# Kernel tuning notes

Measured on AMD Instinct MI355X. Metric: run time of the kernel, lower is better.

## Reference

```python
import jax, jax.numpy as jnp
import numpy as np

NUM_HEADS = 4
NUM_GROUPS = 8
EPS = 1e-5


def group_norm(x, w, b):
    # x: (B, C, H, W); normalize per group of C//NUM_GROUPS channels
    B, C, H, W = x.shape
    xg = x.reshape(B, NUM_GROUPS, C // NUM_GROUPS, H, W)
    mean = xg.mean(axis=(2, 3, 4), keepdims=True)
    var = xg.var(axis=(2, 3, 4), keepdims=True)
    xn = ((xg - mean) * jax.lax.rsqrt(var + EPS)).reshape(B, C, H, W)
    return xn * w[None, :, None, None] + b[None, :, None, None]


def conv1x1(x, w, b):
    # x: (B, C_in, H, W), w: (C_out, C_in), b: (C_out,)
    return jnp.einsum('bchw,oc->bohw', x, w) + b[None, :, None, None]


def setup_inputs() -> dict:
    key = jax.random.key(0)
    B, C, H, W = 4, 256, 64, 64
    k1, k2, k3 = jax.random.split(key, 3)
    scale = 1.0 / np.sqrt(C)
    return {
        'x': jax.random.normal(k1, (B, C, H, W), dtype=jnp.float32),
        'norm_w': jnp.ones((C,), dtype=jnp.float32),
        'norm_b': jnp.zeros((C,), dtype=jnp.float32),
        'qkv_w': jax.random.normal(k2, (3 * C, C), dtype=jnp.float32) * scale,
        'qkv_b': jnp.zeros((3 * C,), dtype=jnp.float32),
        'proj_w': jax.random.normal(k3, (C, C), dtype=jnp.float32) * scale,
        'proj_b': jnp.zeros((C,), dtype=jnp.float32),
    }


def reference(x, norm_w, norm_b, qkv_w, qkv_b, proj_w, proj_b):
    B, C, H, W = x.shape
    hd = C // NUM_HEADS  # head dim
    h = group_norm(x, norm_w, norm_b)
    qkv = conv1x1(h, qkv_w, qkv_b)            # (B, 3C, H, W)
    q, k, v = jnp.split(qkv, 3, axis=1)
    q = q.reshape(B, NUM_HEADS, hd, H * W)
    k = k.reshape(B, NUM_HEADS, hd, H * W)
    v = v.reshape(B, NUM_HEADS, hd, H * W)
    attn = jnp.einsum('bhcn,bhcm->bhnm', q, k) / jnp.sqrt(jnp.asarray(hd, x.dtype))
    attn = jax.nn.softmax(attn, axis=-1)
    out = jnp.einsum('bhnm,bhcm->bhcn', attn, v).reshape(B, C, H, W)
    out = conv1x1(out, proj_w, proj_b)
    return x + out
```

## Files before the change

kernel.cpp:

```cpp
#include <hip/hip_runtime.h>
#include <hip/hip_bf16.h>
#include <stdint.h>


#define B_  4
#define C_  256
#define N_  4096
#define NH_ 4
#define HD_ 64
#define G_  8
#define CPG_ 32
#define GRP_ELEMS (CPG_ * N_)

typedef __attribute__((ext_vector_type(8))) short short8;
typedef __attribute__((ext_vector_type(4))) float f32x4;
typedef __attribute__((ext_vector_type(4))) unsigned short us4;

__device__ __forceinline__ unsigned short f2bf(float f) {
  union { float f; unsigned u; } v; v.f = f;
  unsigned r = v.u + 0x7FFFu + ((v.u >> 16) & 1u);
  return (unsigned short)(r >> 16);
}

__device__ __forceinline__ unsigned pkbf2(float a, float b) {
  __hip_bfloat162 h = __float22bfloat162_rn(make_float2(a, b));
  unsigned r; __builtin_memcpy(&r, &h, sizeof(r)); return r;
}

__device__ __forceinline__ void dma16(const unsigned short* g, unsigned short* l) {
  __builtin_amdgcn_global_load_lds(
      (const __attribute__((address_space(1))) unsigned int*)(g),
      (__attribute__((address_space(3))) unsigned int*)(l), 16, 0, 0);
}

__global__ void gn_partial_cvt(const float* __restrict__ x, float* __restrict__ partial,
                               const float* __restrict__ qkvw, const float* __restrict__ projw,
                               unsigned short* __restrict__ wq, unsigned short* __restrict__ wp) {
  __shared__ float ls[8];
  int t = threadIdx.x;
  if (blockIdx.x >= 512) {
    int i = (blockIdx.x - 512) * 256 + t;
    if (i < 768 * 256) wq[i] = f2bf(qkvw[i]);
    if (i < 256 * 256) wp[i] = f2bf(projw[i]);
    return;
  }
  int idx = blockIdx.x;
  int slice = idx & 15, g = (idx >> 4) & 7, b = idx >> 7;
  const float* base = x + (size_t)(b * C_ + g * CPG_) * N_ + slice * 256;
  float s = 0.f, sq = 0.f;
#pragma unroll
  for (int cc = 0; cc < CPG_; cc++) {
    float v = base[(size_t)cc * N_ + t];
    s += v; sq += v * v;
  }
#pragma unroll
  for (int off = 32; off; off >>= 1) {
    s  += __shfl_down(s,  off, 64);
    sq += __shfl_down(sq, off, 64);
  }
  int wave = t >> 6, lane = t & 63;
  if (lane == 0) { ls[wave * 2] = s; ls[wave * 2 + 1] = sq; }
  __syncthreads();
  if (t == 0) {
    float S = ls[0] + ls[2] + ls[4] + ls[6];
    float SQ = ls[1] + ls[3] + ls[5] + ls[7];
    partial[idx * 2] = S; partial[idx * 2 + 1] = SQ;
  }
}

__global__ void gn_apply(const float* __restrict__ x,
                         const float* __restrict__ nw, const float* __restrict__ nb,
                         const float* __restrict__ partial, unsigned short* __restrict__ hT) {
  int nt = blockIdx.x, ct = blockIdx.y, b = blockIdx.z;
  __shared__ unsigned short tile[32][72];
  int t = threadIdx.x;
  int lane = t & 63;
  int grp = b * G_ + ct;
  float s = 0.f, sq = 0.f;
  if (lane < 16) {
    s  = partial[(grp * 16 + lane) * 2];
    sq = partial[(grp * 16 + lane) * 2 + 1];
  }
#pragma unroll
  for (int off = 8; off; off >>= 1) {
    s  += __shfl_down(s,  off, 64);
    sq += __shfl_down(sq, off, 64);
  }
  s  = __shfl(s,  0, 64);
  sq = __shfl(sq, 0, 64);
  const float inv = 1.0f / (float)GRP_ELEMS;
  float mean = s * inv;
  float rstd = rsqrtf(sq * inv - mean * mean + 1e-5f);

  int n_loc = t & 63, c_loc = t >> 6;
  const float* xb = x + (size_t)(b * C_ + ct * CPG_) * N_ + nt * 64;
#pragma unroll
  for (int rr = 0; rr < 8; rr++) {
    int cc = rr * 4 + c_loc;
    int c = ct * CPG_ + cc;
    float v = xb[(size_t)cc * N_ + n_loc];
    v = (v - mean) * rstd * nw[c] + nb[c];
    tile[cc][n_loc] = f2bf(v);
  }
  __syncthreads();
  int n = t >> 2, c8 = (t & 3) * 8;
  us4 lo, hi;
#pragma unroll
  for (int j = 0; j < 4; j++) lo[j] = tile[c8 + j][n];
#pragma unroll
  for (int j = 0; j < 4; j++) hi[j] = tile[c8 + 4 + j][n];
  unsigned short* outp = hT + ((size_t)(b * N_ + nt * 64 + n)) * C_ + ct * CPG_ + c8;
  *reinterpret_cast<us4*>(outp) = lo;
  *reinterpret_cast<us4*>(outp + 4) = hi;
}

__global__ __launch_bounds__(256) void qkv_gemm(
    const unsigned short* __restrict__ hT, const unsigned short* __restrict__ wq,
    const float* __restrict__ qb,
    unsigned short* __restrict__ Qt, unsigned short* __restrict__ Kt,
    unsigned short* __restrict__ V) {
  int ot = blockIdx.x >> 7;
  int nt = (blockIdx.x & 127) >> 2;
  int b  = blockIdx.x & 3;
  int t = threadIdx.x;
  int wave = t >> 6, lane = t & 63, l15 = lane & 15, quad = lane >> 4, l7 = l15 & 7;

  __shared__ __align__(16) unsigned short sh[128 * C_];
  {
    int row0 = wave * 2 + (lane >> 5);
    int col8 = lane & 31;
    int src8 = (col8 & 24) | ((col8 & 7) ^ (row0 & 7));
    const unsigned short* gsrc = hT + ((size_t)(b * N_ + nt * 128 + row0)) * C_ + src8 * 8;
#pragma unroll
    for (int it = 0; it < 16; it++)
      dma16(gsrc + (size_t)it * 8 * C_, sh + (it * 8 + wave * 2) * C_);
  }

  f32x4 acc[2][8];
#pragma unroll
  for (int r = 0; r < 2; r++)
#pragma unroll
    for (int tt = 0; tt < 8; tt++) acc[r][tt] = (f32x4){0.f, 0.f, 0.f, 0.f};

  const short8* arow[2];
#pragma unroll
  for (int r = 0; r < 2; r++)
    arow[r] = reinterpret_cast<const short8*>(
        wq + (size_t)(ot * 128 + wave * 32 + r * 16 + l15) * C_);

  asm volatile("s_waitcnt vmcnt(0)" ::: "memory");
  __syncthreads();

#pragma unroll
  for (int kk = 0; kk < 8; kk++) {
    int g = kk * 4 + quad;
    int col8 = (g & 24) | ((g & 7) ^ l7);
    short8 bfr[8];
#pragma unroll
    for (int tt = 0; tt < 8; tt++)
      bfr[tt] = *reinterpret_cast<const short8*>(&sh[(tt * 16 + l15) * C_ + col8 * 8]);
#pragma unroll
    for (int r = 0; r < 2; r++) {
      short8 a = arow[r][g];
#pragma unroll
      for (int tt = 0; tt < 8; tt++)
        acc[r][tt] = __builtin_amdgcn_mfma_f32_16x16x32_bf16(a, bfr[tt], acc[r][tt], 0, 0, 0);
    }
  }

  int sec = ot >> 1;
  int head = (ot & 1) * 2 + (wave >> 1);
  int bh = b * NH_ + head;
  const float SC = 0.125f * 1.44269504088896340736f;

#pragma unroll
  for (int r = 0; r < 2; r++) {
    int o_glob = ot * 128 + wave * 32 + r * 16;
    int cw = (o_glob & 63) + quad * 4;
    if (sec == 0) {
#pragma unroll
      for (int tt = 0; tt < 8; tt++) {
        int n = nt * 128 + tt * 16 + l15;
        us4 pk;
#pragma unroll
        for (int i = 0; i < 4; i++)
          pk[i] = f2bf((acc[r][tt][i] + qb[o_glob + quad * 4 + i]) * SC);
        *reinterpret_cast<us4*>(Qt + ((size_t)bh * N_ + n) * HD_ + cw) = pk;
      }
    } else if (sec == 1) {
#pragma unroll
      for (int tt = 0; tt < 8; tt++) {
        int n = nt * 128 + tt * 16 + l15;
        us4 pk;
#pragma unroll
        for (int i = 0; i < 4; i++)
          pk[i] = f2bf(acc[r][tt][i] + qb[o_glob + quad * 4 + i]);
        *reinterpret_cast<us4*>(Kt + ((size_t)bh * N_ + n) * HD_ + cw) = pk;
      }
    } else {
#pragma unroll
      for (int tt = 0; tt < 8; tt++) {
        int n = nt * 128 + tt * 16 + l15;
#pragma unroll
        for (int i = 0; i < 4; i++)
          V[((size_t)bh * HD_ + cw + i) * N_ + n] =
              f2bf(acc[r][tt][i] + qb[o_glob + quad * 4 + i]);
      }
    }
  }
}

__global__ __launch_bounds__(256, 2) void flash_attn(
    const unsigned short* __restrict__ Qt, const unsigned short* __restrict__ Kt,
    const unsigned short* __restrict__ Vv, unsigned short* __restrict__ aoT) {
  int bh = blockIdx.x & 15, qt = blockIdx.x >> 4;
  int b = bh >> 2, head = bh & 3;
  int t = threadIdx.x;
  int wave = t >> 6, lane = t & 63, l15 = lane & 15, quad = lane >> 4;
  int l7 = l15 & 7;
  int qsub = wave >> 1, khalf = wave & 1;

  const unsigned short* Qb = Qt + (size_t)bh * N_ * HD_;
  const unsigned short* Kb = Kt + (size_t)bh * N_ * HD_;
  const unsigned short* Vb = Vv + (size_t)bh * HD_ * N_;
  int q_base = qt * 128 + qsub * 64;

  __shared__ __align__(16) unsigned char smem[65536];
  unsigned short* Ks = (unsigned short*)smem;
  unsigned short* Vs = (unsigned short*)(smem + 32768);
  float* Obuf = (float*)smem;
  float* lbuf = (float*)(smem + 34816);

  const short8 vones = {(short)0x3F80, (short)0x3F80, (short)0x3F80, (short)0x3F80,
                        (short)0x3F80, (short)0x3F80, (short)0x3F80, (short)0x3F80};

  short8 qf[4][2];
#pragma unroll
  for (int r = 0; r < 4; r++)
#pragma unroll
    for (int h = 0; h < 2; h++)
      qf[r][h] = *reinterpret_cast<const short8*>(
          Qb + (size_t)(q_base + r * 16 + l15) * HD_ + h * 32 + quad * 8);

  f32x4 oa[4][4], la[4];
#pragma unroll
  for (int r = 0; r < 4; r++) {
    la[r] = (f32x4){0.f, 0.f, 0.f, 0.f};
#pragma unroll
    for (int ct = 0; ct < 4; ct++) oa[r][ct] = (f32x4){0.f, 0.f, 0.f, 0.f};
  }

  int i8 = lane >> 3, e = lane & 7;
  int perm = (e ^ i8) * 8;
  int kvoff = (khalf * 2) * 4096;
  auto stage = [&](int kt2, int buf) {
    int m0 = khalf * 2048 + kt2 * 64;
    unsigned short* Kd = Ks + kvoff + buf * 4096;
    unsigned short* Vd = Vs + kvoff + buf * 4096;
#pragma unroll
    for (int cc = 0; cc < 4; cc++) {
      int c = qsub * 4 + cc;
      dma16(Kb + (size_t)(m0 + c * 8 + i8) * HD_ + perm, Kd + c * 512);
      dma16(Vb + (size_t)(c * 8 + i8) * N_ + m0 + perm, Vd + c * 512);
    }
  };

  stage(0, 0);

#pragma unroll 1
  for (int kt = 0; kt < 32; kt++) {
    int buf = kt & 1;
    if (kt + 1 < 32) {
      stage(kt + 1, buf ^ 1);
      asm volatile("s_waitcnt vmcnt(8)" ::: "memory");
    } else {
      asm volatile("s_waitcnt vmcnt(0)" ::: "memory");
    }
    __builtin_amdgcn_s_barrier();

    const unsigned short* Kbuf = Ks + kvoff + buf * 4096;
    const unsigned short* Vbuf = Vs + kvoff + buf * 4096;

    short8 kf[4][2], vf[4][2];
#pragma unroll
    for (int tt = 0; tt < 4; tt++)
#pragma unroll
      for (int kh2 = 0; kh2 < 2; kh2++) {
        kf[tt][kh2] = *reinterpret_cast<const short8*>(
            &Kbuf[(tt * 16 + l15) * 64 + (((kh2 * 4 + quad) ^ l7) * 8)]);
        vf[tt][kh2] = *reinterpret_cast<const short8*>(
            &Vbuf[(tt * 16 + l15) * 64 + (((kh2 * 4 + quad) ^ l7) * 8)]);
      }

#pragma unroll
    for (int r = 0; r < 4; r++) {
      f32x4 s[4];
#pragma unroll
      for (int tt = 0; tt < 4; tt++) {
        f32x4 z = (f32x4){0.f, 0.f, 0.f, 0.f};
        z = __builtin_amdgcn_mfma_f32_16x16x32_bf16(kf[tt][0], qf[r][0], z, 0, 0, 0);
        s[tt] = __builtin_amdgcn_mfma_f32_16x16x32_bf16(kf[tt][1], qf[r][1], z, 0, 0, 0);
      }
      unsigned Apk[4], Bpk[4];
#pragma unroll
      for (int tt = 0; tt < 4; tt++) {
        Apk[tt] = pkbf2(__builtin_amdgcn_exp2f(s[tt][0]), __builtin_amdgcn_exp2f(s[tt][1]));
        Bpk[tt] = pkbf2(__builtin_amdgcn_exp2f(s[tt][2]), __builtin_amdgcn_exp2f(s[tt][3]));
      }
      union { unsigned u[4]; short8 v; } f0, f1;
      {
        auto ua = __builtin_amdgcn_permlane32_swap(Apk[0], Apk[1], false, false);
        auto pa = __builtin_amdgcn_permlane16_swap(ua[0], ua[1], false, false);
        auto ub = __builtin_amdgcn_permlane32_swap(Bpk[0], Bpk[1], false, false);
        auto pb = __builtin_amdgcn_permlane16_swap(ub[0], ub[1], false, false);
        f0.u[0] = pa[0]; f0.u[1] = pb[0]; f0.u[2] = pa[1]; f0.u[3] = pb[1];
        auto uc = __builtin_amdgcn_permlane32_swap(Apk[2], Apk[3], false, false);
        auto pc = __builtin_amdgcn_permlane16_swap(uc[0], uc[1], false, false);
        auto ud = __builtin_amdgcn_permlane32_swap(Bpk[2], Bpk[3], false, false);
        auto pd = __builtin_amdgcn_permlane16_swap(ud[0], ud[1], false, false);
        f1.u[0] = pc[0]; f1.u[1] = pd[0]; f1.u[2] = pc[1]; f1.u[3] = pd[1];
      }
      short8 pf0 = f0.v, pf1 = f1.v;
#pragma unroll
      for (int ct = 0; ct < 4; ct++) {
        oa[r][ct] = __builtin_amdgcn_mfma_f32_16x16x32_bf16(vf[ct][0], pf0, oa[r][ct], 0, 0, 0);
        oa[r][ct] = __builtin_amdgcn_mfma_f32_16x16x32_bf16(vf[ct][1], pf1, oa[r][ct], 0, 0, 0);
      }
      la[r] = __builtin_amdgcn_mfma_f32_16x16x32_bf16(vones, pf0, la[r], 0, 0, 0);
      la[r] = __builtin_amdgcn_mfma_f32_16x16x32_bf16(vones, pf1, la[r], 0, 0, 0);
    }
  }

  __builtin_amdgcn_s_barrier();
  if (khalf == 1) {
#pragma unroll
    for (int r = 0; r < 4; r++) {
#pragma unroll
      for (int ct = 0; ct < 4; ct++)
#pragma unroll
        for (int i = 0; i < 4; i++)
          Obuf[qsub * 4352 + (ct * 16 + quad * 4 + i) * 68 + r * 16 + l15] = oa[r][ct][i];
      if (quad == 0) lbuf[qsub * 64 + r * 16 + l15] = la[r][0];
    }
  }
  __builtin_amdgcn_s_barrier();
  if (khalf == 0) {
#pragma unroll
    for (int r = 0; r < 4; r++) {
      float inv = 1.0f / (la[r][0] + lbuf[qsub * 64 + r * 16 + l15]);
      int n = q_base + r * 16 + l15;
#pragma unroll
      for (int ct = 0; ct < 4; ct++) {
        const float* ob = &Obuf[qsub * 4352 + (ct * 16 + quad * 4) * 68 + r * 16 + l15];
        union { unsigned u2[2]; us4 v; } w;
        w.u2[0] = pkbf2((oa[r][ct][0] + ob[0]) * inv, (oa[r][ct][1] + ob[68]) * inv);
        w.u2[1] = pkbf2((oa[r][ct][2] + ob[136]) * inv, (oa[r][ct][3] + ob[204]) * inv);
        *reinterpret_cast<us4*>(
            aoT + ((size_t)(b * N_ + n)) * C_ + head * HD_ + ct * 16 + quad * 4) = w.v;
      }
    }
  }
}

__global__ __launch_bounds__(256) void proj_gemm(
    const unsigned short* __restrict__ aoT, const unsigned short* __restrict__ wp,
    const float* __restrict__ pb, const float* __restrict__ x,
    float* __restrict__ out) {
  int ot = blockIdx.x >> 7;
  int nt = (blockIdx.x & 127) >> 2;
  int b  = blockIdx.x & 3;
  int t = threadIdx.x;
  int wave = t >> 6, lane = t & 63, l15 = lane & 15, quad = lane >> 4, l7 = l15 & 7;
  int o_base = ot * 64 + wave * 16;

  __shared__ __align__(16) unsigned short sh[128 * C_];
  {
    int row0 = wave * 2 + (lane >> 5);
    int col8 = lane & 31;
    int src8 = (col8 & 24) | ((col8 & 7) ^ (row0 & 7));
    const unsigned short* gsrc = aoT + ((size_t)(b * N_ + nt * 128 + row0)) * C_ + src8 * 8;
#pragma unroll
    for (int it = 0; it < 16; it++)
      dma16(gsrc + (size_t)it * 8 * C_, sh + (it * 8 + wave * 2) * C_);
  }

  f32x4 acc[8];
#pragma unroll
  for (int tt = 0; tt < 8; tt++) acc[tt] = (f32x4){0.f, 0.f, 0.f, 0.f};

  const short8* arow = reinterpret_cast<const short8*>(wp + (size_t)(o_base + l15) * C_);

  asm volatile("s_waitcnt vmcnt(0)" ::: "memory");
  __syncthreads();

#pragma unroll
  for (int kk = 0; kk < 8; kk++) {
    short8 a = arow[kk * 4 + quad];
    int g = kk * 4 + quad;
    int col8 = (g & 24) | ((g & 7) ^ l7);
#pragma unroll
    for (int tt = 0; tt < 8; tt++) {
      short8 bf = *reinterpret_cast<const short8*>(&sh[(tt * 16 + l15) * C_ + col8 * 8]);
      acc[tt] = __builtin_amdgcn_mfma_f32_16x16x32_bf16(a, bf, acc[tt], 0, 0, 0);
    }
  }
#pragma unroll
  for (int tt = 0; tt < 8; tt++) {
    int n = nt * 128 + tt * 16 + l15;
#pragma unroll
    for (int i = 0; i < 4; i++) {
      int o = o_base + quad * 4 + i;
      size_t idx = ((size_t)(b * C_ + o)) * N_ + n;
      out[idx] = acc[tt][i] + pb[o] + x[idx];
    }
  }
}

extern "C" void kernel_launch(void* const* d_in, const int* in_sizes, int n_in,
                              void* d_out, int out_size, void* d_ws, size_t ws_size,
                              hipStream_t stream) {
  const float* x      = (const float*)d_in[0];
  const float* norm_w = (const float*)d_in[1];
  const float* norm_b = (const float*)d_in[2];
  const float* qkv_w  = (const float*)d_in[3];
  const float* qkv_b  = (const float*)d_in[4];
  const float* proj_w = (const float*)d_in[5];
  const float* proj_b = (const float*)d_in[6];
  float* out = (float*)d_out;

  char* ws = (char*)d_ws;
  size_t off = 0;
  auto alloc = [&](size_t bytes) { size_t o = off; off = (off + bytes + 255) & ~(size_t)255; return o; };
  size_t off_partial = alloc(512 * 2 * sizeof(float));
  size_t off_stats   = alloc(32 * 2 * sizeof(float));
  size_t off_wq      = alloc((size_t)768 * 256 * 2);
  size_t off_wp      = alloc((size_t)256 * 256 * 2);
  size_t off_hT      = alloc((size_t)B_ * N_ * C_ * 2);
  size_t off_Qt      = alloc((size_t)B_ * NH_ * N_ * HD_ * 2);
  size_t off_Kt      = alloc((size_t)B_ * NH_ * N_ * HD_ * 2);
  size_t off_V       = alloc((size_t)B_ * NH_ * HD_ * N_ * 2);
  size_t off_aoT     = alloc((size_t)B_ * N_ * C_ * 2);
  (void)off_stats;

  float* partial = (float*)(ws + off_partial);
  unsigned short* wq  = (unsigned short*)(ws + off_wq);
  unsigned short* wp  = (unsigned short*)(ws + off_wp);
  unsigned short* hT  = (unsigned short*)(ws + off_hT);
  unsigned short* Qt  = (unsigned short*)(ws + off_Qt);
  unsigned short* Kt  = (unsigned short*)(ws + off_Kt);
  unsigned short* V   = (unsigned short*)(ws + off_V);
  unsigned short* aoT = (unsigned short*)(ws + off_aoT);

  gn_partial_cvt<<<1280, 256, 0, stream>>>(x, partial, qkv_w, proj_w, wq, wp);
  gn_apply<<<dim3(64, 8, 4), 256, 0, stream>>>(x, norm_w, norm_b, partial, hT);
  qkv_gemm<<<768, 256, 0, stream>>>(hT, wq, qkv_b, Qt, Kt, V);
  flash_attn<<<512, 256, 0, stream>>>(Qt, Kt, V, aoT);
  proj_gemm<<<512, 256, 0, stream>>>(aoT, wp, proj_b, x, out);
}
```

Before: 186.0 us.

## Split flash attention by query rows per wave instead of splitting the KV range

Each wave now owns 32 query rows and walks the whole key/value sequence, replacing the previous scheme where wave pairs split the KV range in halves and merged partial outputs through shared memory. This removes the LDS reduction, the extra barriers and the larger shared buffer (64KB down to 32KB), which may allow more resident blocks. In exchange each wave has fewer rows of work per KV tile, so K/V fragments loaded from LDS are reused across fewer MFMAs, and the loop has twice as many iterations and barriers.

```diff
diff --git a/kernel.cpp b/kernel.cpp
--- a/kernel.cpp
+++ b/kernel.cpp
@@ -218,33 +218,29 @@
   int t = threadIdx.x;
   int wave = t >> 6, lane = t & 63, l15 = lane & 15, quad = lane >> 4;
   int l7 = l15 & 7;
-  int qsub = wave >> 1, khalf = wave & 1;
 
   const unsigned short* Qb = Qt + (size_t)bh * N_ * HD_;
   const unsigned short* Kb = Kt + (size_t)bh * N_ * HD_;
   const unsigned short* Vb = Vv + (size_t)bh * HD_ * N_;
-  int q_base = qt * 128 + qsub * 64;
-
-  __shared__ __align__(16) unsigned char smem[65536];
-  unsigned short* Ks = (unsigned short*)smem;
-  unsigned short* Vs = (unsigned short*)(smem + 32768);
-  float* Obuf = (float*)smem;
-  float* lbuf = (float*)(smem + 34816);
+  int q_base = qt * 128 + wave * 32;
+
+  __shared__ __align__(16) unsigned short KV[2][2][4096];
 
   const short8 vones = {(short)0x3F80, (short)0x3F80, (short)0x3F80, (short)0x3F80,
                         (short)0x3F80, (short)0x3F80, (short)0x3F80, (short)0x3F80};
-
-  short8 qf[4][2];
-#pragma unroll
-  for (int r = 0; r < 4; r++)
+  const f32x4 fzero = (f32x4){0.f, 0.f, 0.f, 0.f};
+
+  short8 qf[2][2];
+#pragma unroll
+  for (int r = 0; r < 2; r++)
 #pragma unroll
     for (int h = 0; h < 2; h++)
       qf[r][h] = *reinterpret_cast<const short8*>(
           Qb + (size_t)(q_base + r * 16 + l15) * HD_ + h * 32 + quad * 8);
 
-  f32x4 oa[4][4], la[4];
-#pragma unroll
-  for (int r = 0; r < 4; r++) {
+  f32x4 oa[2][4], la[2];
+#pragma unroll
+  for (int r = 0; r < 2; r++) {
     la[r] = (f32x4){0.f, 0.f, 0.f, 0.f};
 #pragma unroll
     for (int ct = 0; ct < 4; ct++) oa[r][ct] = (f32x4){0.f, 0.f, 0.f, 0.f};
@@ -252,14 +248,13 @@
 
   int i8 = lane >> 3, e = lane & 7;
   int perm = (e ^ i8) * 8;
-  int kvoff = (khalf * 2) * 4096;
   auto stage = [&](int kt2, int buf) {
-    int m0 = khalf * 2048 + kt2 * 64;
-    unsigned short* Kd = Ks + kvoff + buf * 4096;
-    unsigned short* Vd = Vs + kvoff + buf * 4096;
-#pragma unroll
-    for (int cc = 0; cc < 4; cc++) {
-      int c = qsub * 4 + cc;
+    int m0 = kt2 * 64;
+    unsigned short* Kd = &KV[0][buf][0];
+    unsigned short* Vd = &KV[1][buf][0];
+#pragma unroll
+    for (int cc = 0; cc < 2; cc++) {
+      int c = wave * 2 + cc;
       dma16(Kb + (size_t)(m0 + c * 8 + i8) * HD_ + perm, Kd + c * 512);
       dma16(Vb + (size_t)(c * 8 + i8) * N_ + m0 + perm, Vd + c * 512);
     }
@@ -268,18 +263,18 @@
   stage(0, 0);
 
 #pragma unroll 1
-  for (int kt = 0; kt < 32; kt++) {
+  for (int kt = 0; kt < 64; kt++) {
     int buf = kt & 1;
-    if (kt + 1 < 32) {
+    if (kt + 1 < 64) {
       stage(kt + 1, buf ^ 1);
-      asm volatile("s_waitcnt vmcnt(8)" ::: "memory");
+      asm volatile("s_waitcnt vmcnt(4)" ::: "memory");
     } else {
       asm volatile("s_waitcnt vmcnt(0)" ::: "memory");
     }
     __builtin_amdgcn_s_barrier();
 
-    const unsigned short* Kbuf = Ks + kvoff + buf * 4096;
-    const unsigned short* Vbuf = Vs + kvoff + buf * 4096;
+    const unsigned short* Kbuf = &KV[0][buf][0];
+    const unsigned short* Vbuf = &KV[1][buf][0];
 
     short8 kf[4][2], vf[4][2];
 #pragma unroll
@@ -293,12 +288,11 @@
       }
 
 #pragma unroll
-    for (int r = 0; r < 4; r++) {
+    for (int r = 0; r < 2; r++) {
       f32x4 s[4];
 #pragma unroll
       for (int tt = 0; tt < 4; tt++) {
-        f32x4 z = (f32x4){0.f, 0.f, 0.f, 0.f};
-        z = __builtin_amdgcn_mfma_f32_16x16x32_bf16(kf[tt][0], qf[r][0], z, 0, 0, 0);
+        f32x4 z = __builtin_amdgcn_mfma_f32_16x16x32_bf16(kf[tt][0], qf[r][0], fzero, 0, 0, 0);
         s[tt] = __builtin_amdgcn_mfma_f32_16x16x32_bf16(kf[tt][1], qf[r][1], z, 0, 0, 0);
       }
       unsigned Apk[4], Bpk[4];
@@ -331,33 +325,17 @@
     }
   }
 
-  __builtin_amdgcn_s_barrier();
-  if (khalf == 1) {
-#pragma unroll
-    for (int r = 0; r < 4; r++) {
-#pragma unroll
-      for (int ct = 0; ct < 4; ct++)
-#pragma unroll
-        for (int i = 0; i < 4; i++)
-          Obuf[qsub * 4352 + (ct * 16 + quad * 4 + i) * 68 + r * 16 + l15] = oa[r][ct][i];
-      if (quad == 0) lbuf[qsub * 64 + r * 16 + l15] = la[r][0];
-    }
-  }
-  __builtin_amdgcn_s_barrier();
-  if (khalf == 0) {
-#pragma unroll
-    for (int r = 0; r < 4; r++) {
-      float inv = 1.0f / (la[r][0] + lbuf[qsub * 64 + r * 16 + l15]);
-      int n = q_base + r * 16 + l15;
-#pragma unroll
-      for (int ct = 0; ct < 4; ct++) {
-        const float* ob = &Obuf[qsub * 4352 + (ct * 16 + quad * 4) * 68 + r * 16 + l15];
-        union { unsigned u2[2]; us4 v; } w;
-        w.u2[0] = pkbf2((oa[r][ct][0] + ob[0]) * inv, (oa[r][ct][1] + ob[68]) * inv);
-        w.u2[1] = pkbf2((oa[r][ct][2] + ob[136]) * inv, (oa[r][ct][3] + ob[204]) * inv);
-        *reinterpret_cast<us4*>(
-            aoT + ((size_t)(b * N_ + n)) * C_ + head * HD_ + ct * 16 + quad * 4) = w.v;
-      }
+#pragma unroll
+  for (int r = 0; r < 2; r++) {
+    float inv = 1.0f / la[r][0];
+    int n = q_base + r * 16 + l15;
+#pragma unroll
+    for (int ct = 0; ct < 4; ct++) {
+      union { unsigned u2[2]; us4 v; } w;
+      w.u2[0] = pkbf2(oa[r][ct][0] * inv, oa[r][ct][1] * inv);
+      w.u2[1] = pkbf2(oa[r][ct][2] * inv, oa[r][ct][3] * inv);
+      *reinterpret_cast<us4*>(
+          aoT + ((size_t)(b * N_ + n)) * C_ + head * HD_ + ct * 16 + quad * 4) = w.v;
     }
   }
 }
```

Result: no change. 188.0 us (+1.0%).
